# Optimization experiments

Measured on AMD Instinct MI355X. Metric: run time of the kernel, lower is better.

Reference implementation:

```python
import jax, jax.numpy as jnp
import numpy as np

SOBEL_X = jnp.array([[-1., 0., 1.], [-2., 0., 2.], [-1., 0., 1.]], dtype=jnp.float32).reshape(1, 1, 3, 3)
SOBEL_Y = jnp.array([[-1., -2., -1.], [0., 0., 0.], [1., 2., 1.]], dtype=jnp.float32).reshape(1, 1, 3, 3)
LAPLACE = jnp.array([[-1., -1., -1.], [-1., 8., -1.], [-1., -1., -1.]], dtype=jnp.float32).reshape(1, 1, 3, 3)


def _conv3x3(img, kernel):
    # img: [B,1,H,W], kernel: [1,1,3,3]; zero padding 1, stride 1 (matches F.conv2d)
    return jax.lax.conv_general_dilated(
        img, kernel, window_strides=(1, 1), padding=((1, 1), (1, 1)),
        dimension_numbers=("NCHW", "OIHW", "NCHW"))


def _charbonnier(s):
    return jnp.sqrt(s * s + jnp.float32(0.001) ** 2)


def setup_inputs() -> dict:
    key = jax.random.key(0)
    k1, k2 = jax.random.split(key)
    B, C, H, W = 64, 1, 512, 512
    pred = jax.random.uniform(k1, (B, C, H, W), dtype=jnp.float32)
    target = jax.random.uniform(k2, (B, C, H, W), dtype=jnp.float32)
    return {"pred": pred, "target": target}


def reference(pred, target):
    alpha = jnp.float32(10.0)
    s1 = jnp.float32(10.0)
    s2 = jnp.float32(1.0)

    sal_x = jnp.abs(_conv3x3(pred, SOBEL_X))
    sal_y = jnp.abs(_conv3x3(pred, SOBEL_Y))
    gt_x = _conv3x3(target, SOBEL_X)
    gt_y = _conv3x3(target, SOBEL_Y)
    w_x = jnp.exp(jnp.abs(gt_x) * -alpha)
    w_y = jnp.exp(jnp.abs(gt_y) * -alpha)
    cps_xy = _charbonnier(sal_x * w_x) + _charbonnier(sal_y * w_y)

    lap_sal = jnp.abs(_conv3x3(pred, LAPLACE))
    lap_gt = jnp.abs(_conv3x3(target, LAPLACE))
    weighted_lap = _charbonnier(lap_sal * jnp.exp(lap_gt * -alpha))

    return s1 * jnp.mean(cps_xy) + s2 * jnp.mean(weighted_lap)
```

## Files before the change

### kernel.cpp

```cpp
#include <hip/hip_runtime.h>
#include <math.h>

#define IMG_W 512
#define IMG_H 512
#define RPT 8
#define STRIPS (IMG_H / RPT)
#define IMG_PX (IMG_H * IMG_W)

#if __has_builtin(__builtin_amdgcn_exp2f)
#define EXP2F(x) __builtin_amdgcn_exp2f(x)
#else
#define EXP2F(x) exp2f(x)
#endif
#if __has_builtin(__builtin_amdgcn_sqrtf)
#define SQRTF(x) __builtin_amdgcn_sqrtf(x)
#else
#define SQRTF(x) sqrtf(x)
#endif

#define NEG10_LOG2E (-14.426950408889634f)

__device__ __forceinline__ float2 mk2(float a, float b) { float2 r; r.x = a; r.y = b; return r; }
__device__ __forceinline__ float2 add2(float2 a, float2 b) { return mk2(a.x + b.x, a.y + b.y); }
__device__ __forceinline__ float2 sub2(float2 a, float2 b) { return mk2(a.x - b.x, a.y - b.y); }
__device__ __forceinline__ float2 fma2c(float k, float2 a, float2 b) {
    return mk2(fmaf(k, a.x, b.x), fmaf(k, a.y, b.y));
}

struct Rw { float2 d, t, s; };

__device__ __forceinline__ Rw make_dst(float4 v, bool eL, bool eR) {
    const float lx = eL ? 0.f : v.x;
    const float rw = eR ? 0.f : v.w;
    const float2 L = mk2(lx,  v.y);
    const float2 C = mk2(v.y, v.z);
    const float2 R = mk2(v.z, rw);
    Rw w;
    w.d = sub2(R, L);
    w.s = add2(add2(L, R), C);
    w.t = add2(w.s, C);
    return w;
}

__device__ __forceinline__ Rw zero_dst() {
    Rw w; w.d = mk2(0.f, 0.f); w.t = mk2(0.f, 0.f); w.s = mk2(0.f, 0.f); return w;
}

__global__ __launch_bounds__(256, 4) void loss_partial_kernel(
        const float* __restrict__ pred, const float* __restrict__ targ,
        float* __restrict__ partial, int nimg) {
    const int strip = blockIdx.x & (STRIPS - 1);
    const int b     = blockIdx.x >> 6;
    const int x0    = threadIdx.x << 1;
    const int y0    = strip * RPT;
    const bool eL = (x0 == 0);
    const bool eR = (x0 == IMG_W - 2);
    const int nmax = nimg * IMG_PX - 4;
    const bool lastStrip = (strip == STRIPS - 1);

    const int rowIdx = b * IMG_PX + y0 * IMG_W + (x0 - 1);

    const float eps2 = 1e-6f;

    Rw pa, pb, ta, tb;
    if (strip == 0) {
        pa = zero_dst(); ta = zero_dst();
    } else {
        pa = make_dst(*(const float4*)(pred + rowIdx - IMG_W), eL, eR);
        ta = make_dst(*(const float4*)(targ + rowIdx - IMG_W), eL, eR);
    }
    {
        const int ic = max(rowIdx, 0);
        pb = make_dst(*(const float4*)(pred + ic), eL, eR);
        tb = make_dst(*(const float4*)(targ + ic), eL, eR);
    }

    float4 rp = *(const float4*)(pred + rowIdx + IMG_W);
    float4 rt = *(const float4*)(targ + rowIdx + IMG_W);

    float sXY = 0.f, sL = 0.f;
#pragma unroll
    for (int i = 0; i < RPT; ++i) {
        float4 rp2, rt2;
        if (i < RPT - 1) {
            const int ip = min(rowIdx + (i + 2) * IMG_W, nmax);
            rp2 = *(const float4*)(pred + ip);
            rt2 = *(const float4*)(targ + ip);
        }

        Rw pc, tc;
        if (i == RPT - 1 && lastStrip) {
            pc = zero_dst(); tc = zero_dst();
        } else {
            pc = make_dst(rp, eL, eR);
            tc = make_dst(rt, eL, eR);
        }

        const float2 sxp = add2(fma2c(2.f, pb.d, pa.d), pc.d);
        const float2 syp = sub2(pc.t, pa.t);
        const float2 nsp = add2(add2(pa.s, pb.s), pc.s);
        const float2 lpp = fma2c(9.f, sub2(pb.t, pb.s), mk2(-nsp.x, -nsp.y));

        const float2 sxt = add2(fma2c(2.f, tb.d, ta.d), tc.d);
        const float2 syt = sub2(tc.t, ta.t);
        const float2 nst = add2(add2(ta.s, tb.s), tc.s);
        const float2 lpt = fma2c(9.f, sub2(tb.t, tb.s), mk2(-nst.x, -nst.y));

        {
            const float ax = fabsf(sxp.x) * EXP2F(fabsf(sxt.x) * NEG10_LOG2E);
            const float ay = fabsf(syp.x) * EXP2F(fabsf(syt.x) * NEG10_LOG2E);
            const float al = fabsf(lpp.x) * EXP2F(fabsf(lpt.x) * NEG10_LOG2E);
            sXY += SQRTF(fmaf(ax, ax, eps2)) + SQRTF(fmaf(ay, ay, eps2));
            sL  += SQRTF(fmaf(al, al, eps2));
        }
        {
            const float ax = fabsf(sxp.y) * EXP2F(fabsf(sxt.y) * NEG10_LOG2E);
            const float ay = fabsf(syp.y) * EXP2F(fabsf(syt.y) * NEG10_LOG2E);
            const float al = fabsf(lpp.y) * EXP2F(fabsf(lpt.y) * NEG10_LOG2E);
            sXY += SQRTF(fmaf(ax, ax, eps2)) + SQRTF(fmaf(ay, ay, eps2));
            sL  += SQRTF(fmaf(al, al, eps2));
        }

        pa = pb; pb = pc;
        ta = tb; tb = tc;
        rp = rp2; rt = rt2;
    }

    float sum = fmaf(10.f, sXY, sL);

#pragma unroll
    for (int off = 32; off > 0; off >>= 1) sum += __shfl_down(sum, off, 64);
    __shared__ float ws[4];
    const int lane = threadIdx.x & 63, wid = threadIdx.x >> 6;
    if (lane == 0) ws[wid] = sum;
    __syncthreads();
    if (threadIdx.x == 0) partial[blockIdx.x] = ws[0] + ws[1] + ws[2] + ws[3];
}

__global__ __launch_bounds__(256) void loss_final_kernel(
        const float* __restrict__ partial, int n, float* __restrict__ out, float scale) {
    float s = 0.f;
    for (int i = threadIdx.x; i < n; i += 256) s += partial[i];
#pragma unroll
    for (int off = 32; off > 0; off >>= 1) s += __shfl_down(s, off, 64);
    __shared__ float ws[4];
    const int lane = threadIdx.x & 63, wid = threadIdx.x >> 6;
    if (lane == 0) ws[wid] = s;
    __syncthreads();
    if (threadIdx.x == 0) out[0] = (ws[0] + ws[1] + ws[2] + ws[3]) * scale;
}

extern "C" void kernel_launch(void* const* d_in, const int* in_sizes, int n_in,
                              void* d_out, int out_size, void* d_ws, size_t ws_size,
                              hipStream_t stream) {
    const float* pred = (const float*)d_in[0];
    const float* targ = (const float*)d_in[1];
    float* out = (float*)d_out;
    float* partial = (float*)d_ws;

    const int total = in_sizes[0];
    const int B = total / (IMG_H * IMG_W);
    const int nblocks = B * STRIPS;

    loss_partial_kernel<<<nblocks, 256, 0, stream>>>(pred, targ, partial, B);
    const float scale = 1.0f / (float)total;
    loss_final_kernel<<<1, 256, 0, stream>>>(partial, nblocks, out, scale);
}
```

Measured before the change: 36.08 us.

## Stage strip rows into LDS via direct global-to-LDS loads

Each block now copies its 10-row strip (including halo rows) of both images into shared memory with global_load_lds, and zero-fills out-of-bounds rows. Threads then read their overlapping 4-wide windows from LDS instead of issuing overlapping unaligned float4 global loads per row. This removes redundant, misaligned global traffic and the per-row prefetch logic. In exchange it adds a roughly 41 KB LDS footprint per block, which may limit occupancy, plus a full wait and barrier before any compute can start, so load and compute no longer overlap.

After: 44.67 us. 1.24x slower.

```diff
diff --git a/kernel.cpp b/kernel.cpp
--- a/kernel.cpp
+++ b/kernel.cpp
@@ -6,6 +6,8 @@
 #define RPT 8
 #define STRIPS (IMG_H / RPT)
 #define IMG_PX (IMG_H * IMG_W)
+#define LROWS (RPT + 2)
+#define LSTRIDE 516
 
 #if __has_builtin(__builtin_amdgcn_exp2f)
 #define EXP2F(x) __builtin_amdgcn_exp2f(x)
@@ -42,59 +44,61 @@
     return w;
 }
 
-__device__ __forceinline__ Rw zero_dst() {
-    Rw w; w.d = mk2(0.f, 0.f); w.t = mk2(0.f, 0.f); w.s = mk2(0.f, 0.f); return w;
-}
-
 __global__ __launch_bounds__(256, 4) void loss_partial_kernel(
         const float* __restrict__ pred, const float* __restrict__ targ,
-        float* __restrict__ partial, int nimg) {
+        float* __restrict__ partial) {
+    __shared__ float lds[2][LROWS][LSTRIDE];
+
     const int strip = blockIdx.x & (STRIPS - 1);
     const int b     = blockIdx.x >> 6;
-    const int x0    = threadIdx.x << 1;
+    const int w     = threadIdx.x >> 6;
+    const int l     = threadIdx.x & 63;
     const int y0    = strip * RPT;
-    const bool eL = (x0 == 0);
-    const bool eR = (x0 == IMG_W - 2);
-    const int nmax = nimg * IMG_PX - 4;
-    const bool lastStrip = (strip == STRIPS - 1);
 
-    const int rowIdx = b * IMG_PX + y0 * IMG_W + (x0 - 1);
+#pragma unroll
+    for (int j = 0; j < 10; ++j) {
+        const int cid  = j * 4 + w;
+        const int img  = (cid >= 20) ? 1 : 0;
+        const int rem  = cid - img * 20;
+        const int r    = rem >> 1;
+        const int half = rem & 1;
+        const int y    = y0 - 1 + r;
+        float* ldst = &lds[img][r][1 + half * 256];
+        if ((unsigned)y < (unsigned)IMG_H) {
+            const float* gsrc = (img ? targ : pred)
+                + (size_t)b * IMG_PX + (size_t)y * IMG_W + half * 256 + l * 4;
+            __builtin_amdgcn_global_load_lds(
+                (__attribute__((address_space(1))) const void*)gsrc,
+                (__attribute__((address_space(3))) void*)ldst, 16, 0, 0);
+        } else {
+            float* z = ldst + l * 4;
+            z[0] = 0.f; z[1] = 0.f; z[2] = 0.f; z[3] = 0.f;
+        }
+    }
+    asm volatile("s_waitcnt vmcnt(0)" ::: "memory");
+    __syncthreads();
 
+    const int x0 = threadIdx.x << 1;
+    const bool eL = (threadIdx.x == 0);
+    const bool eR = (threadIdx.x == 255);
     const float eps2 = 1e-6f;
 
-    Rw pa, pb, ta, tb;
-    if (strip == 0) {
-        pa = zero_dst(); ta = zero_dst();
-    } else {
-        pa = make_dst(*(const float4*)(pred + rowIdx - IMG_W), eL, eR);
-        ta = make_dst(*(const float4*)(targ + rowIdx - IMG_W), eL, eR);
-    }
-    {
-        const int ic = max(rowIdx, 0);
-        pb = make_dst(*(const float4*)(pred + ic), eL, eR);
-        tb = make_dst(*(const float4*)(targ + ic), eL, eR);
-    }
+    #define QUAD(imgI, rI) ({                                   \
+        const float* _row = &lds[(imgI)][(rI)][x0];             \
+        const float2 _a = *(const float2*)(_row);               \
+        const float2 _c = *(const float2*)(_row + 2);           \
+        float4 _v; _v.x = _a.x; _v.y = _a.y; _v.z = _c.x; _v.w = _c.y; _v; })
 
-    float4 rp = *(const float4*)(pred + rowIdx + IMG_W);
-    float4 rt = *(const float4*)(targ + rowIdx + IMG_W);
+    Rw pa = make_dst(QUAD(0, 0), eL, eR);
+    Rw ta = make_dst(QUAD(1, 0), eL, eR);
+    Rw pb = make_dst(QUAD(0, 1), eL, eR);
+    Rw tb = make_dst(QUAD(1, 1), eL, eR);
 
     float sXY = 0.f, sL = 0.f;
 #pragma unroll
     for (int i = 0; i < RPT; ++i) {
-        float4 rp2, rt2;
-        if (i < RPT - 1) {
-            const int ip = min(rowIdx + (i + 2) * IMG_W, nmax);
-            rp2 = *(const float4*)(pred + ip);
-            rt2 = *(const float4*)(targ + ip);
-        }
-
-        Rw pc, tc;
-        if (i == RPT - 1 && lastStrip) {
-            pc = zero_dst(); tc = zero_dst();
-        } else {
-            pc = make_dst(rp, eL, eR);
-            tc = make_dst(rt, eL, eR);
-        }
+        Rw pc = make_dst(QUAD(0, i + 2), eL, eR);
+        Rw tc = make_dst(QUAD(1, i + 2), eL, eR);
 
         const float2 sxp = add2(fma2c(2.f, pb.d, pa.d), pc.d);
         const float2 syp = sub2(pc.t, pa.t);
@@ -123,7 +127,6 @@
 
         pa = pb; pb = pc;
         ta = tb; tb = tc;
-        rp = rp2; rt = rt2;
     }
 
     float sum = fmaf(10.f, sXY, sL);
@@ -131,8 +134,7 @@
 #pragma unroll
     for (int off = 32; off > 0; off >>= 1) sum += __shfl_down(sum, off, 64);
     __shared__ float ws[4];
-    const int lane = threadIdx.x & 63, wid = threadIdx.x >> 6;
-    if (lane == 0) ws[wid] = sum;
+    if (l == 0) ws[w] = sum;
     __syncthreads();
     if (threadIdx.x == 0) partial[blockIdx.x] = ws[0] + ws[1] + ws[2] + ws[3];
 }
@@ -162,7 +164,7 @@
     const int B = total / (IMG_H * IMG_W);
     const int nblocks = B * STRIPS;
 
-    loss_partial_kernel<<<nblocks, 256, 0, stream>>>(pred, targ, partial, B);
+    loss_partial_kernel<<<nblocks, 256, 0, stream>>>(pred, targ, partial);
     const float scale = 1.0f / (float)total;
     loss_final_kernel<<<1, 256, 0, stream>>>(partial, nblocks, out, scale);
 }
```
